# Kernel tuning notes

Hardware: AMD Instinct MI355X
Metric: run time of the kernel (lower is better)

The kernel has to match this reference:

```python
import jax, jax.numpy as jnp
import numpy as np

ALPHA = 0.1
BETA = float(np.log(1.0 / 4.0 + 1.0))  # lambda_=1, layer=4

N_NODES = 50000
N_EDGES = 600000
D = 128


def setup_inputs() -> dict:
    key = jax.random.key(0)
    k1, k2, k3, k4, k5 = jax.random.split(key, 5)
    feat = jax.random.normal(k1, (N_NODES, D), dtype=jnp.float32)
    feat_0 = jax.random.normal(k2, (N_NODES, D), dtype=jnp.float32)
    weight1 = jax.random.normal(k3, (D, D), dtype=jnp.float32)  # nn.init.normal_
    bias = jnp.zeros((D,), dtype=jnp.float32)
    src = jax.random.randint(k4, (N_EDGES,), 0, N_NODES, dtype=jnp.int32)
    dst = jax.random.randint(k5, (N_EDGES,), 0, N_NODES, dtype=jnp.int32)
    return {"feat": feat, "feat_0": feat_0, "weight1": weight1, "bias": bias,
            "src": src, "dst": dst}


def reference(feat, feat_0, weight1, bias, src, dst):
    n = feat.shape[0]
    # symmetric normalization: D^{-1/2} A_hat D^{-1/2} using in-degrees, clamped at 1
    deg = jax.ops.segment_sum(jnp.ones(dst.shape[0], dtype=feat.dtype), dst,
                              num_segments=n)
    norm = jnp.clip(deg, 1.0)[:, None] ** -0.5  # [N, 1]
    h = feat * norm
    agg = jax.ops.segment_sum(h[src], dst, num_segments=n)  # copy_u + sum
    agg = agg * norm
    # initial residual blend (torch does feat.add_(feat_0) in-place -> blended h
    # feeds both terms of the addmm)
    h = agg * (1.0 - ALPHA) + feat_0 * ALPHA
    # identity mapping: (1-beta)*h + beta*(h @ W1), plus bias
    rst = (1.0 - BETA) * h + BETA * (h @ weight1) + bias
    return rst
```

## Files before the change

### kernel.cpp

```cpp
#include <hip/hip_runtime.h>

static constexpr int   N_NODES = 50000;
static constexpr int   N_EDGES = 600000;
static constexpr int   D       = 128;
static constexpr int   CAP     = 64;
static constexpr float ALPHA   = 0.1f;
static constexpr float BETA    = 0.22314355131420976f;
static constexpr float OMB     = 1.0f - BETA;

static constexpr int TMF = 64;
static constexpr int NTF = (N_NODES + TMF - 1) / TMF;
static constexpr int HP  = 132;

typedef __attribute__((ext_vector_type(8))) short short8;
typedef __attribute__((ext_vector_type(4))) float f32x4;

__device__ __forceinline__ unsigned int f2bf(float f) {
    unsigned int u = __float_as_uint(f);
    return (u + 0x7FFFu + ((u >> 16) & 1u)) >> 16;
}
__device__ __forceinline__ float bf2f(unsigned int b) {
    return __uint_as_float(b << 16);
}
__device__ __forceinline__ float deg2norm(int d) {
    return rsqrtf(fmaxf((float)d, 1.0f));
}

__global__ void conv_kernel(const float* __restrict__ feat,
                            unsigned short* __restrict__ featb,
                            const float* __restrict__ W,
                            unsigned short* __restrict__ wbt,
                            int* __restrict__ cnt) {
    const int tid = blockIdx.x * blockDim.x + threadIdx.x;
    if (tid * 4 < N_NODES)
        *reinterpret_cast<int4*>(cnt + tid * 4) = make_int4(0, 0, 0, 0);
    if (tid * 8 < D * D) {
        const int c  = (tid * 8) >> 7;
        const int k0 = (tid * 8) & 127;
        unsigned short w8[8];
        #pragma unroll
        for (int j = 0; j < 8; ++j)
            w8[j] = (unsigned short)f2bf(W[(size_t)(k0 + j) * D + c]);
        #pragma unroll
        for (int j = 0; j < 8; ++j)
            wbt[(size_t)c * D + k0 + j] = w8[j];
    }
    const size_t e0 = (size_t)tid * 16;
    if (e0 < (size_t)N_NODES * D) {
        const float* p = feat + e0;
        #pragma unroll
        for (int q = 0; q < 2; ++q) {
            float4 a = *reinterpret_cast<const float4*>(p + q * 8);
            float4 b = *reinterpret_cast<const float4*>(p + q * 8 + 4);
            uint4 o;
            o.x = f2bf(a.x) | (f2bf(a.y) << 16);
            o.y = f2bf(a.z) | (f2bf(a.w) << 16);
            o.z = f2bf(b.x) | (f2bf(b.y) << 16);
            o.w = f2bf(b.z) | (f2bf(b.w) << 16);
            *reinterpret_cast<uint4*>(featb + e0 + q * 8) = o;
        }
    }
}

__global__ void fill_kernel(const int* __restrict__ src, const int* __restrict__ dst,
                            int* __restrict__ cnt, int* __restrict__ slots) {
    const int tid = blockIdx.x * blockDim.x + threadIdx.x;
    if (tid < N_EDGES) {
        int s = src[tid];
        int d = dst[tid];
        int p = atomicAdd(&cnt[d], 1);
        if (p < CAP) slots[d * CAP + p] = s;
    }
}

__global__ __launch_bounds__(256) void gather_kernel(
    const unsigned short* __restrict__ featb, const int* __restrict__ slots,
    const int* __restrict__ cnt_arr, float* __restrict__ agg) {
    const int node = blockIdx.x * 4 + (threadIdx.x >> 6);
    const int lane = threadIdx.x & 63;
    const int half = lane >> 5;
    const int l32  = lane & 31;
    if (node >= N_NODES) return;
    const int base = node * CAP;
    const int cnt  = min(cnt_arr[node], CAP);
    const unsigned short* __restrict__ fcol = featb + (size_t)l32 * 4;

    int   s_l = 0;
    float n_l = 0.0f;
    if (lane < cnt) {
        s_l = slots[base + lane];
        n_l = deg2norm(cnt_arr[s_l]);
    }

    float4 acc = make_float4(0.f, 0.f, 0.f, 0.f);
    const int nb = (cnt + 7) >> 3;
    for (int b = 0; b < nb; ++b) {
        const int j = b * 8 + half;
        int   s0 = __shfl(s_l, j);      float n0 = __shfl(n_l, j);
        int   s1 = __shfl(s_l, j + 2);  float n1 = __shfl(n_l, j + 2);
        int   s2 = __shfl(s_l, j + 4);  float n2 = __shfl(n_l, j + 4);
        int   s3 = __shfl(s_l, j + 6);  float n3 = __shfl(n_l, j + 6);
        ushort4 u0 = *reinterpret_cast<const ushort4*>(fcol + (size_t)s0 * D);
        ushort4 u1 = *reinterpret_cast<const ushort4*>(fcol + (size_t)s1 * D);
        ushort4 u2 = *reinterpret_cast<const ushort4*>(fcol + (size_t)s2 * D);
        ushort4 u3 = *reinterpret_cast<const ushort4*>(fcol + (size_t)s3 * D);
        acc.x += bf2f(u0.x)*n0 + bf2f(u1.x)*n1 + bf2f(u2.x)*n2 + bf2f(u3.x)*n3;
        acc.y += bf2f(u0.y)*n0 + bf2f(u1.y)*n1 + bf2f(u2.y)*n2 + bf2f(u3.y)*n3;
        acc.z += bf2f(u0.z)*n0 + bf2f(u1.z)*n1 + bf2f(u2.z)*n2 + bf2f(u3.z)*n3;
        acc.w += bf2f(u0.w)*n0 + bf2f(u1.w)*n1 + bf2f(u2.w)*n2 + bf2f(u3.w)*n3;
    }
    acc.x += __shfl_xor(acc.x, 32);
    acc.y += __shfl_xor(acc.y, 32);
    acc.z += __shfl_xor(acc.z, 32);
    acc.w += __shfl_xor(acc.w, 32);
    if (half == 0)
        *reinterpret_cast<float4*>(agg + (size_t)node * D + l32 * 4) = acc;
}

__global__ __launch_bounds__(256, 2) void final_kernel(
    const float* __restrict__ feat_0,
    const unsigned short* __restrict__ wbt,
    const float* __restrict__ bias,
    const int* __restrict__ cnt_arr,
    float* __restrict__ out)
{
    __shared__ float h_sh[TMF * HP];

    const int t    = threadIdx.x;
    const int row0 = blockIdx.x * TMF;

    #pragma unroll
    for (int i = 0; i < 8; ++i) {
        int idx  = (i * 256 + t) * 4;
        int r    = idx >> 7;
        int c    = idx & 127;
        int node = row0 + r;
        float4 h = make_float4(0.f, 0.f, 0.f, 0.f);
        if (node < N_NODES) {
            float nm = deg2norm(cnt_arr[node]) * (1.0f - ALPHA);
            float4 a  = *reinterpret_cast<const float4*>(out    + (size_t)node * D + c);
            float4 f0 = *reinterpret_cast<const float4*>(feat_0 + (size_t)node * D + c);
            h.x = a.x * nm + f0.x * ALPHA;
            h.y = a.y * nm + f0.y * ALPHA;
            h.z = a.z * nm + f0.z * ALPHA;
            h.w = a.w * nm + f0.w * ALPHA;
        }
        *reinterpret_cast<float4*>(&h_sh[r * HP + c]) = h;
    }
    __syncthreads();

    const int wave = t >> 6;
    const int lane = t & 63;
    const int lrow = lane & 15;
    const int lgrp = lane >> 4;
    const int cb   = wave * 32;

    short8 bfrag[2][4];
    #pragma unroll
    for (int ct = 0; ct < 2; ++ct) {
        const int col = cb + ct * 16 + lrow;
        #pragma unroll
        for (int kb = 0; kb < 4; ++kb)
            bfrag[ct][kb] = *reinterpret_cast<const short8*>(
                wbt + (size_t)col * D + kb * 32 + lgrp * 8);
    }

    f32x4 acc[4][2];
    #pragma unroll
    for (int rt = 0; rt < 4; ++rt)
        #pragma unroll
        for (int ct = 0; ct < 2; ++ct)
            acc[rt][ct] = (f32x4){0.f, 0.f, 0.f, 0.f};

    #pragma unroll
    for (int rt = 0; rt < 4; ++rt) {
        const float* hp = &h_sh[(rt * 16 + lrow) * HP];
        short8 afrag[4];
        #pragma unroll
        for (int kb = 0; kb < 4; ++kb) {
            float4 x = *reinterpret_cast<const float4*>(hp + kb * 32 + lgrp * 8);
            float4 y = *reinterpret_cast<const float4*>(hp + kb * 32 + lgrp * 8 + 4);
            short8 a;
            a[0] = (short)f2bf(x.x); a[1] = (short)f2bf(x.y);
            a[2] = (short)f2bf(x.z); a[3] = (short)f2bf(x.w);
            a[4] = (short)f2bf(y.x); a[5] = (short)f2bf(y.y);
            a[6] = (short)f2bf(y.z); a[7] = (short)f2bf(y.w);
            afrag[kb] = a;
        }
        #pragma unroll
        for (int ct = 0; ct < 2; ++ct)
            #pragma unroll
            for (int kb = 0; kb < 4; ++kb)
                acc[rt][ct] = __builtin_amdgcn_mfma_f32_16x16x32_bf16(
                    afrag[kb], bfrag[ct][kb], acc[rt][ct], 0, 0, 0);
    }

    #pragma unroll
    for (int ct = 0; ct < 2; ++ct) {
        const int col = cb + ct * 16 + lrow;
        const float bv = bias[col];
        #pragma unroll
        for (int rt = 0; rt < 4; ++rt) {
            #pragma unroll
            for (int reg = 0; reg < 4; ++reg) {
                const int lr   = rt * 16 + lgrp * 4 + reg;
                const int node = row0 + lr;
                if (node < N_NODES) {
                    float h = h_sh[lr * HP + col];
                    out[(size_t)node * D + col] =
                        OMB * h + BETA * acc[rt][ct][reg] + bv;
                }
            }
        }
    }
}

extern "C" void kernel_launch(void* const* d_in, const int* in_sizes, int n_in,
                              void* d_out, int out_size, void* d_ws, size_t ws_size,
                              hipStream_t stream) {
    const float* feat   = (const float*)d_in[0];
    const float* feat_0 = (const float*)d_in[1];
    const float* W      = (const float*)d_in[2];
    const float* bias   = (const float*)d_in[3];
    const int*   src    = (const int*)d_in[4];
    const int*   dst    = (const int*)d_in[5];
    float*       out    = (float*)d_out;

    char* ws = (char*)d_ws;
    int*   cnt   = (int*)ws;            ws += (size_t)N_NODES * 4;
    int*   slots = (int*)ws;            ws += (size_t)N_NODES * CAP * 4;
    unsigned short* featb = (unsigned short*)ws;  ws += (size_t)N_NODES * D * 2;
    unsigned short* wbt   = (unsigned short*)ws;

    conv_kernel<<<(N_NODES * (D / 16) + 255) / 256, 256, 0, stream>>>(
        feat, featb, W, wbt, cnt);

    fill_kernel<<<(N_EDGES + 255) / 256, 256, 0, stream>>>(src, dst, cnt, slots);

    gather_kernel<<<(N_NODES + 3) / 4, 256, 0, stream>>>(featb, slots, cnt, out);

    final_kernel<<<NTF, 256, 0, stream>>>(feat_0, wbt, bias, cnt, out);
}
```

Before: 181.0 us.

## Fuse neighbor gather into the residual GEMM kernel via shared memory

Merges the gather kernel and the final GEMM kernel into one kernel. Each 512-thread block gathers 32 nodes, with 4 per wave, and writes the blended h straight into shared memory, then runs the MFMA identity-mapping GEMM on that tile. This removes the fp32 agg write and read-back through global memory and one kernel launch. In exchange, each block waits on a __syncthreads after an irregular gather, and the W fragments are reloaded by more blocks because the tiles are now smaller.

Measured after the change: 177.3 us. -2.0%, faster.

```diff
diff --git a/kernel.cpp b/kernel.cpp
--- a/kernel.cpp
+++ b/kernel.cpp
@@ -8,7 +8,7 @@
 static constexpr float BETA    = 0.22314355131420976f;
 static constexpr float OMB     = 1.0f - BETA;
 
-static constexpr int TMF = 64;
+static constexpr int TMF = 32;
 static constexpr int NTF = (N_NODES + TMF - 1) / TMF;
 static constexpr int HP  = 132;
 
@@ -73,107 +73,92 @@
     }
 }
 
-__global__ __launch_bounds__(256) void gather_kernel(
+__global__ __launch_bounds__(512, 4) void gf2_kernel(
     const unsigned short* __restrict__ featb, const int* __restrict__ slots,
-    const int* __restrict__ cnt_arr, float* __restrict__ agg) {
-    const int node = blockIdx.x * 4 + (threadIdx.x >> 6);
-    const int lane = threadIdx.x & 63;
-    const int half = lane >> 5;
-    const int l32  = lane & 31;
-    if (node >= N_NODES) return;
-    const int base = node * CAP;
-    const int cnt  = min(cnt_arr[node], CAP);
-    const unsigned short* __restrict__ fcol = featb + (size_t)l32 * 4;
-
-    int   s_l = 0;
-    float n_l = 0.0f;
-    if (lane < cnt) {
-        s_l = slots[base + lane];
-        n_l = deg2norm(cnt_arr[s_l]);
-    }
-
-    float4 acc = make_float4(0.f, 0.f, 0.f, 0.f);
-    const int nb = (cnt + 7) >> 3;
-    for (int b = 0; b < nb; ++b) {
-        const int j = b * 8 + half;
-        int   s0 = __shfl(s_l, j);      float n0 = __shfl(n_l, j);
-        int   s1 = __shfl(s_l, j + 2);  float n1 = __shfl(n_l, j + 2);
-        int   s2 = __shfl(s_l, j + 4);  float n2 = __shfl(n_l, j + 4);
-        int   s3 = __shfl(s_l, j + 6);  float n3 = __shfl(n_l, j + 6);
-        ushort4 u0 = *reinterpret_cast<const ushort4*>(fcol + (size_t)s0 * D);
-        ushort4 u1 = *reinterpret_cast<const ushort4*>(fcol + (size_t)s1 * D);
-        ushort4 u2 = *reinterpret_cast<const ushort4*>(fcol + (size_t)s2 * D);
-        ushort4 u3 = *reinterpret_cast<const ushort4*>(fcol + (size_t)s3 * D);
-        acc.x += bf2f(u0.x)*n0 + bf2f(u1.x)*n1 + bf2f(u2.x)*n2 + bf2f(u3.x)*n3;
-        acc.y += bf2f(u0.y)*n0 + bf2f(u1.y)*n1 + bf2f(u2.y)*n2 + bf2f(u3.y)*n3;
-        acc.z += bf2f(u0.z)*n0 + bf2f(u1.z)*n1 + bf2f(u2.z)*n2 + bf2f(u3.z)*n3;
-        acc.w += bf2f(u0.w)*n0 + bf2f(u1.w)*n1 + bf2f(u2.w)*n2 + bf2f(u3.w)*n3;
-    }
-    acc.x += __shfl_xor(acc.x, 32);
-    acc.y += __shfl_xor(acc.y, 32);
-    acc.z += __shfl_xor(acc.z, 32);
-    acc.w += __shfl_xor(acc.w, 32);
-    if (half == 0)
-        *reinterpret_cast<float4*>(agg + (size_t)node * D + l32 * 4) = acc;
-}
-
-__global__ __launch_bounds__(256, 2) void final_kernel(
-    const float* __restrict__ feat_0,
+    const int* __restrict__ cnt_arr, const float* __restrict__ feat_0,
     const unsigned short* __restrict__ wbt,
     const float* __restrict__ bias,
-    const int* __restrict__ cnt_arr,
     float* __restrict__ out)
 {
     __shared__ float h_sh[TMF * HP];
 
     const int t    = threadIdx.x;
-    const int row0 = blockIdx.x * TMF;
-
-    #pragma unroll
-    for (int i = 0; i < 8; ++i) {
-        int idx  = (i * 256 + t) * 4;
-        int r    = idx >> 7;
-        int c    = idx & 127;
-        int node = row0 + r;
-        float4 h = make_float4(0.f, 0.f, 0.f, 0.f);
-        if (node < N_NODES) {
-            float nm = deg2norm(cnt_arr[node]) * (1.0f - ALPHA);
-            float4 a  = *reinterpret_cast<const float4*>(out    + (size_t)node * D + c);
-            float4 f0 = *reinterpret_cast<const float4*>(feat_0 + (size_t)node * D + c);
-            h.x = a.x * nm + f0.x * ALPHA;
-            h.y = a.y * nm + f0.y * ALPHA;
-            h.z = a.z * nm + f0.z * ALPHA;
-            h.w = a.w * nm + f0.w * ALPHA;
-        }
-        *reinterpret_cast<float4*>(&h_sh[r * HP + c]) = h;
-    }
-    __syncthreads();
-
     const int wave = t >> 6;
     const int lane = t & 63;
+    const int half = lane >> 5;
+    const int l32  = lane & 31;
+    const int row0 = blockIdx.x * TMF;
+    const unsigned short* __restrict__ fcol = featb + (size_t)l32 * 4;
+
+    #pragma unroll 1
+    for (int i = 0; i < 4; ++i) {
+        const int lr   = wave * 4 + i;
+        const int node = row0 + lr;
+        if (node < N_NODES) {
+            const int base = node * CAP;
+            const int cnt  = min(cnt_arr[node], CAP);
+
+            int   s_l = 0;
+            float n_l = 0.0f;
+            if (lane < cnt) {
+                s_l = slots[base + lane];
+                n_l = deg2norm(cnt_arr[s_l]);
+            }
+
+            float4 acc = make_float4(0.f, 0.f, 0.f, 0.f);
+            const int nb = (cnt + 7) >> 3;
+            for (int b = 0; b < nb; ++b) {
+                const int j = b * 8 + half;
+                int   s0 = __shfl(s_l, j);      float n0 = __shfl(n_l, j);
+                int   s1 = __shfl(s_l, j + 2);  float n1 = __shfl(n_l, j + 2);
+                int   s2 = __shfl(s_l, j + 4);  float n2 = __shfl(n_l, j + 4);
+                int   s3 = __shfl(s_l, j + 6);  float n3 = __shfl(n_l, j + 6);
+                ushort4 u0 = *reinterpret_cast<const ushort4*>(fcol + (size_t)s0 * D);
+                ushort4 u1 = *reinterpret_cast<const ushort4*>(fcol + (size_t)s1 * D);
+                ushort4 u2 = *reinterpret_cast<const ushort4*>(fcol + (size_t)s2 * D);
+                ushort4 u3 = *reinterpret_cast<const ushort4*>(fcol + (size_t)s3 * D);
+                acc.x += bf2f(u0.x)*n0 + bf2f(u1.x)*n1 + bf2f(u2.x)*n2 + bf2f(u3.x)*n3;
+                acc.y += bf2f(u0.y)*n0 + bf2f(u1.y)*n1 + bf2f(u2.y)*n2 + bf2f(u3.y)*n3;
+                acc.z += bf2f(u0.z)*n0 + bf2f(u1.z)*n1 + bf2f(u2.z)*n2 + bf2f(u3.z)*n3;
+                acc.w += bf2f(u0.w)*n0 + bf2f(u1.w)*n1 + bf2f(u2.w)*n2 + bf2f(u3.w)*n3;
+            }
+            acc.x += __shfl_xor(acc.x, 32);
+            acc.y += __shfl_xor(acc.y, 32);
+            acc.z += __shfl_xor(acc.z, 32);
+            acc.w += __shfl_xor(acc.w, 32);
+            if (half == 0) {
+                float nm = deg2norm(cnt_arr[node]) * (1.0f - ALPHA);
+                float4 f0 = *reinterpret_cast<const float4*>(
+                                feat_0 + (size_t)node * D + l32 * 4);
+                float4 h;
+                h.x = acc.x * nm + f0.x * ALPHA;
+                h.y = acc.y * nm + f0.y * ALPHA;
+                h.z = acc.z * nm + f0.z * ALPHA;
+                h.w = acc.w * nm + f0.w * ALPHA;
+                *reinterpret_cast<float4*>(&h_sh[lr * HP + l32 * 4]) = h;
+            }
+        } else if (half == 0) {
+            *reinterpret_cast<float4*>(&h_sh[lr * HP + l32 * 4]) =
+                make_float4(0.f, 0.f, 0.f, 0.f);
+        }
+    }
+    __syncthreads();
+
     const int lrow = lane & 15;
     const int lgrp = lane >> 4;
-    const int cb   = wave * 32;
-
-    short8 bfrag[2][4];
+    const int col  = wave * 16 + lrow;
+
+    short8 bfrag[4];
     #pragma unroll
-    for (int ct = 0; ct < 2; ++ct) {
-        const int col = cb + ct * 16 + lrow;
-        #pragma unroll
-        for (int kb = 0; kb < 4; ++kb)
-            bfrag[ct][kb] = *reinterpret_cast<const short8*>(
-                wbt + (size_t)col * D + kb * 32 + lgrp * 8);
-    }
-
-    f32x4 acc[4][2];
+    for (int kb = 0; kb < 4; ++kb)
+        bfrag[kb] = *reinterpret_cast<const short8*>(
+            wbt + (size_t)col * D + kb * 32 + lgrp * 8);
+
+    f32x4 acc0 = (f32x4){0.f, 0.f, 0.f, 0.f};
+    f32x4 acc1 = (f32x4){0.f, 0.f, 0.f, 0.f};
+
     #pragma unroll
-    for (int rt = 0; rt < 4; ++rt)
-        #pragma unroll
-        for (int ct = 0; ct < 2; ++ct)
-            acc[rt][ct] = (f32x4){0.f, 0.f, 0.f, 0.f};
-
-    #pragma unroll
-    for (int rt = 0; rt < 4; ++rt) {
+    for (int rt = 0; rt < 2; ++rt) {
         const float* hp = &h_sh[(rt * 16 + lrow) * HP];
         short8 afrag[4];
         #pragma unroll
@@ -187,29 +172,36 @@
             a[6] = (short)f2bf(y.z); a[7] = (short)f2bf(y.w);
             afrag[kb] = a;
         }
-        #pragma unroll
-        for (int ct = 0; ct < 2; ++ct)
+        if (rt == 0) {
             #pragma unroll
             for (int kb = 0; kb < 4; ++kb)
-                acc[rt][ct] = __builtin_amdgcn_mfma_f32_16x16x32_bf16(
-                    afrag[kb], bfrag[ct][kb], acc[rt][ct], 0, 0, 0);
-    }
-
+                acc0 = __builtin_amdgcn_mfma_f32_16x16x32_bf16(
+                    afrag[kb], bfrag[kb], acc0, 0, 0, 0);
+        } else {
+            #pragma unroll
+            for (int kb = 0; kb < 4; ++kb)
+                acc1 = __builtin_amdgcn_mfma_f32_16x16x32_bf16(
+                    afrag[kb], bfrag[kb], acc1, 0, 0, 0);
+        }
+    }
+
+    const float bv = bias[col];
     #pragma unroll
-    for (int ct = 0; ct < 2; ++ct) {
-        const int col = cb + ct * 16 + lrow;
-        const float bv = bias[col];
-        #pragma unroll
-        for (int rt = 0; rt < 4; ++rt) {
-            #pragma unroll
-            for (int reg = 0; reg < 4; ++reg) {
-                const int lr   = rt * 16 + lgrp * 4 + reg;
-                const int node = row0 + lr;
-                if (node < N_NODES) {
-                    float h = h_sh[lr * HP + col];
-                    out[(size_t)node * D + col] =
-                        OMB * h + BETA * acc[rt][ct][reg] + bv;
-                }
+    for (int reg = 0; reg < 4; ++reg) {
+        {
+            const int lr   = lgrp * 4 + reg;
+            const int node = row0 + lr;
+            if (node < N_NODES) {
+                float h = h_sh[lr * HP + col];
+                out[(size_t)node * D + col] = OMB * h + BETA * acc0[reg] + bv;
+            }
+        }
+        {
+            const int lr   = 16 + lgrp * 4 + reg;
+            const int node = row0 + lr;
+            if (node < N_NODES) {
+                float h = h_sh[lr * HP + col];
+                out[(size_t)node * D + col] = OMB * h + BETA * acc1[reg] + bv;
             }
         }
     }
@@ -237,7 +229,5 @@
 
     fill_kernel<<<(N_EDGES + 255) / 256, 256, 0, stream>>>(src, dst, cnt, slots);
 
-    gather_kernel<<<(N_NODES + 3) / 4, 256, 0, stream>>>(featb, slots, cnt, out);
-
-    final_kernel<<<NTF, 256, 0, stream>>>(feat_0, wbt, bias, cnt, out);
-}
+    gf2_kernel<<<NTF, 512, 0, stream>>>(featb, slots, cnt, feat_0, wbt, bias, out);
+}
```
